# Kernel tuning notes

Measured on AMD Instinct MI355X. Metric: run time of the kernel, lower is better.

The kernel has to match this reference:

```python
import jax, jax.numpy as jnp
import numpy as np

DIM = 768
NUM_HEADS = 16
HEAD_DIM = DIM // NUM_HEADS


def setup_inputs() -> dict:
    key = jax.random.key(0)
    ks = jax.random.split(key, 9)
    B, S = 8, 1024
    s = 1.0 / np.sqrt(DIM)
    return {
        "x": jax.random.normal(ks[0], (B, S, DIM), dtype=jnp.float32),
        "Wq": jax.random.normal(ks[1], (DIM, DIM), dtype=jnp.float32) * s,
        "bq": jnp.zeros((DIM,), dtype=jnp.float32),
        "Wk": jax.random.normal(ks[2], (DIM, DIM), dtype=jnp.float32) * s,
        "bk": jnp.zeros((DIM,), dtype=jnp.float32),
        "Wv": jax.random.normal(ks[3], (DIM, DIM), dtype=jnp.float32) * s,
        "bv": jnp.zeros((DIM,), dtype=jnp.float32),
        "Wo": jax.random.normal(ks[4], (DIM, DIM), dtype=jnp.float32) * s,
        "bo": jnp.zeros((DIM,), dtype=jnp.float32),
    }


def reference(x, Wq, bq, Wk, bk, Wv, bv, Wo, bo):
    # x: [B, S, D]. Dropout in eval mode (identity).
    B, S, D = x.shape
    H, Hd = NUM_HEADS, HEAD_DIM
    # projections -> [B, H, S, Hd]
    q = (x @ Wq + bq).reshape(B, S, H, Hd).transpose(0, 2, 1, 3)
    k = (x @ Wk + bk).reshape(B, S, H, Hd).transpose(0, 2, 1, 3)
    v = (x @ Wv + bv).reshape(B, S, H, Hd).transpose(0, 2, 1, 3)
    scores = jnp.einsum('bhqd,bhkd->bhqk', q, k) / jnp.sqrt(jnp.asarray(Hd, x.dtype))
    attn = jax.nn.softmax(scores, axis=-1)
    out = jnp.einsum('bhqk,bhkd->bhqd', attn, v)  # [B, H, S, Hd]
    out = out.transpose(0, 2, 1, 3).reshape(B, S, D)
    return out @ Wo + bo
```

## Files before the change

kernel.cpp:

```cpp
#include <hip/hip_runtime.h>
#include <hip/hip_bf16.h>
#include <math.h>

#define DIM 768
#define HEADS 16
#define HD 48
#define BATCH 8
#define SEQ 1024
#define M_TOTAL (BATCH * SEQ)

using short8 = __attribute__((ext_vector_type(8))) short;
using f32x4 = __attribute__((ext_vector_type(4))) float;
using ushort8 = __attribute__((ext_vector_type(8))) unsigned short;
using ushort4v = __attribute__((ext_vector_type(4))) unsigned short;

__device__ __forceinline__ unsigned short f2bf(float f) {
    unsigned int u = __float_as_uint(f);
    u = u + 0x7FFFu + ((u >> 16) & 1u);
    return (unsigned short)(u >> 16);
}

__device__ __forceinline__ void load16_lds(const void* g, void* l) {
    __builtin_amdgcn_global_load_lds(
        (const __attribute__((address_space(1))) unsigned int*)g,
        (__attribute__((address_space(3))) unsigned int*)l, 16, 0, 0);
}

__device__ __forceinline__ ushort4v pk4bf(const f32x4 v) {
    union { __hip_bfloat162 h2[2]; ushort4v u4; } cv;
    cv.h2[0] = __float22bfloat162_rn(make_float2(v[0], v[1]));
    cv.h2[1] = __float22bfloat162_rn(make_float2(v[2], v[3]));
    return cv.u4;
}

__device__ __forceinline__ short8 cat44(ushort4v lo, ushort4v hi) {
    short8 r;
    r[0] = lo[0]; r[1] = lo[1]; r[2] = lo[2]; r[3] = lo[3];
    r[4] = hi[0]; r[5] = hi[1]; r[6] = hi[2]; r[7] = hi[3];
    return r;
}

__global__ __launch_bounds__(256)
void convert_bf16_kernel(const float* __restrict__ in, unsigned short* __restrict__ out) {
    const int idx = blockIdx.x * 256 + threadIdx.x;
    const float4* p = (const float4*)in + (size_t)idx * 2;
    const float4 a = p[0], b = p[1];
    ushort8 o;
    o[0] = f2bf(a.x); o[1] = f2bf(a.y); o[2] = f2bf(a.z); o[3] = f2bf(a.w);
    o[4] = f2bf(b.x); o[5] = f2bf(b.y); o[6] = f2bf(b.z); o[7] = f2bf(b.w);
    *((ushort8*)out + idx) = o;
}

__global__ __launch_bounds__(256)
void fill_vt_ones_kernel(unsigned short* __restrict__ vt) {
    const int g = blockIdx.x * 256 + threadIdx.x;
    const int bh = g >> 11;
    const int within = g & 2047;
    ushort8 o;
#pragma unroll
    for (int i = 0; i < 8; ++i) o[i] = 0x3F80;
    *(ushort8*)(vt + (size_t)bh * 65536 + 49152 + within * 8) = o;
}

__global__ __launch_bounds__(256)
void convert_w4_kernel(const float* __restrict__ W0, const float* __restrict__ W1,
                       const float* __restrict__ W2, const float* __restrict__ W3,
                       unsigned short* __restrict__ O0, unsigned short* __restrict__ O1,
                       unsigned short* __restrict__ O2, unsigned short* __restrict__ O3) {
    const float* W;
    unsigned short* O;
    switch (blockIdx.z) {
        case 0: W = W0; O = O0; break;
        case 1: W = W1; O = O1; break;
        case 2: W = W2; O = O2; break;
        default: W = W3; O = O3; break;
    }
    __shared__ unsigned short tile[32][33];
    const int t = threadIdx.x;
    const int r = t >> 3;
    const int c4 = (t & 7) * 4;
    {
        const float4 v = *(const float4*)(W + (size_t)(blockIdx.x * 32 + r) * DIM + blockIdx.y * 32 + c4);
        tile[r][c4 + 0] = f2bf(v.x);
        tile[r][c4 + 1] = f2bf(v.y);
        tile[r][c4 + 2] = f2bf(v.z);
        tile[r][c4 + 3] = f2bf(v.w);
    }
    __syncthreads();
    ushort4v o;
    o[0] = tile[c4 + 0][r];
    o[1] = tile[c4 + 1][r];
    o[2] = tile[c4 + 2][r];
    o[3] = tile[c4 + 3][r];
    *(ushort4v*)(O + (size_t)(blockIdx.y * 32 + r) * DIM + blockIdx.x * 32 + c4) = o;
}

__global__ __launch_bounds__(256)
void gemm_qkv_kernel(const unsigned short* __restrict__ A,
                     const unsigned short* __restrict__ Bt,
                     const float* __restrict__ bq, const float* __restrict__ bk,
                     const float* __restrict__ bv,
                     unsigned short* __restrict__ qp, unsigned short* __restrict__ kp,
                     unsigned short* __restrict__ vt) {
    __shared__ unsigned short As[128 * 32];
    __shared__ unsigned short Bs[128 * 32];

    const int tid = threadIdx.x;
    const int lane = tid & 63;
    const int w = tid >> 6;
    const int quad = lane >> 4;
    const int l15 = lane & 15;
    const int wr = (w >> 1) * 64;
    const int wc = (w & 1) * 64;
    const int row0 = blockIdx.x * 128;
    const int col0g = blockIdx.y * 128;

    const int sr = lane >> 2;
    const int sb = (lane & 3) * 16;

    f32x4 acc[4][4];
    const f32x4 zero = {0.f, 0.f, 0.f, 0.f};
#pragma unroll
    for (int i = 0; i < 4; ++i)
#pragma unroll
        for (int j = 0; j < 4; ++j) acc[i][j] = zero;

    const char* Abase = (const char*)A + (size_t)(row0 + 32 * w + sr) * (DIM * 2) + sb;
    const char* Bbase = (const char*)Bt + (size_t)(col0g + 32 * w + sr) * (DIM * 2) + sb;
    unsigned short* Al = As + w * 1024;
    unsigned short* Bl = Bs + w * 1024;

    for (int k0 = 0; k0 < DIM; k0 += 32) {
        __syncthreads();
        {
            const size_t kb = (size_t)k0 * 2;
            load16_lds(Abase + kb, Al);
            load16_lds(Abase + kb + (size_t)16 * DIM * 2, Al + 512);
            load16_lds(Bbase + kb, Bl);
            load16_lds(Bbase + kb + (size_t)16 * DIM * 2, Bl + 512);
        }
        __syncthreads();

        short8 af[4], bf[4];
        const int koff = quad * 8;
#pragma unroll
        for (int i = 0; i < 4; ++i)
            af[i] = *(const short8*)(As + (wr + 16 * i + l15) * 32 + koff);
#pragma unroll
        for (int j = 0; j < 4; ++j)
            bf[j] = *(const short8*)(Bs + (wc + 16 * j + l15) * 32 + koff);
#pragma unroll
        for (int i = 0; i < 4; ++i)
#pragma unroll
            for (int j = 0; j < 4; ++j)
                acc[i][j] = __builtin_amdgcn_mfma_f32_16x16x32_bf16(af[i], bf[j], acc[i][j], 0, 0, 0);
    }

    const int mat = blockIdx.y / 6;
    const int colbase = (blockIdx.y % 6) * 128;
    const float* bias = (mat == 0) ? bq : (mat == 1) ? bk : bv;
    const float sc = (mat == 0) ? (0.14433756729740643f * 1.4426950408889634f) : 1.0f;
#pragma unroll
    for (int j = 0; j < 4; ++j) {
        const int col = colbase + wc + 16 * j + l15;
        const float bj = bias[col];
        const int h = col / 48;
        const int d = col - h * 48;
        if (mat != 2) {
            unsigned short* outp = (mat == 0) ? qp : kp;
#pragma unroll
            for (int i = 0; i < 4; ++i) {
                const int row = row0 + wr + 16 * i + quad * 4;
#pragma unroll
                for (int r = 0; r < 4; ++r) {
                    const int b = (row + r) >> 10;
                    const int s = (row + r) & 1023;
                    outp[(((size_t)(b * 16 + h) * 1024 + s) << 6) + d] = f2bf((acc[i][j][r] + bj) * sc);
                }
            }
        } else {
#pragma unroll
            for (int i = 0; i < 4; ++i) {
                const int row = row0 + wr + 16 * i + quad * 4;
                const int b = row >> 10;
                const int s = row & 1023;
                ushort4v pk;
#pragma unroll
                for (int r = 0; r < 4; ++r) pk[r] = f2bf(acc[i][j][r] + bj);
                *(ushort4v*)&vt[(((size_t)(b * 16 + h) * 64 + d) << 10) + s] = pk;
            }
        }
    }
}

__global__ __launch_bounds__(256)
void gemm_out_kernel(const unsigned short* __restrict__ A,
                     const unsigned short* __restrict__ Bt,
                     const float* __restrict__ bias,
                     float* __restrict__ Out) {
    __shared__ unsigned short As[128 * 32];
    __shared__ unsigned short Bs[128 * 32];

    const int tid = threadIdx.x;
    const int lane = tid & 63;
    const int w = tid >> 6;
    const int quad = lane >> 4;
    const int l15 = lane & 15;
    const int wr = (w >> 1) * 64;
    const int wc = (w & 1) * 64;
    const int row0 = blockIdx.x * 128;
    const int col0 = blockIdx.y * 128;

    const int sr = lane >> 2;
    const int sb = (lane & 3) * 16;

    f32x4 acc[4][4];
    const f32x4 zero = {0.f, 0.f, 0.f, 0.f};
#pragma unroll
    for (int i = 0; i < 4; ++i)
#pragma unroll
        for (int j = 0; j < 4; ++j) acc[i][j] = zero;

    const char* Abase = (const char*)A + (size_t)(row0 + 32 * w + sr) * (DIM * 2) + sb;
    const char* Bbase = (const char*)Bt + (size_t)(col0 + 32 * w + sr) * (DIM * 2) + sb;
    unsigned short* Al = As + w * 1024;
    unsigned short* Bl = Bs + w * 1024;

    for (int k0 = 0; k0 < DIM; k0 += 32) {
        __syncthreads();
        {
            const size_t kb = (size_t)k0 * 2;
            load16_lds(Abase + kb, Al);
            load16_lds(Abase + kb + (size_t)16 * DIM * 2, Al + 512);
            load16_lds(Bbase + kb, Bl);
            load16_lds(Bbase + kb + (size_t)16 * DIM * 2, Bl + 512);
        }
        __syncthreads();

        short8 af[4], bf[4];
        const int koff = quad * 8;
#pragma unroll
        for (int i = 0; i < 4; ++i)
            af[i] = *(const short8*)(As + (wr + 16 * i + l15) * 32 + koff);
#pragma unroll
        for (int j = 0; j < 4; ++j)
            bf[j] = *(const short8*)(Bs + (wc + 16 * j + l15) * 32 + koff);
#pragma unroll
        for (int i = 0; i < 4; ++i)
#pragma unroll
            for (int j = 0; j < 4; ++j)
                acc[i][j] = __builtin_amdgcn_mfma_f32_16x16x32_bf16(af[i], bf[j], acc[i][j], 0, 0, 0);
    }

#pragma unroll
    for (int j = 0; j < 4; ++j) {
        const int col = col0 + wc + 16 * j + l15;
        const float bj = bias[col];
#pragma unroll
        for (int i = 0; i < 4; ++i) {
            const int row = row0 + wr + 16 * i + quad * 4;
#pragma unroll
            for (int r = 0; r < 4; ++r)
                Out[(size_t)(row + r) * DIM + col] = acc[i][j][r] + bj;
        }
    }
}

__global__ __launch_bounds__(256, 4)
void attn_mfma_kernel(const unsigned short* __restrict__ qp,
                      const unsigned short* __restrict__ kp,
                      const unsigned short* __restrict__ vt,
                      unsigned short* __restrict__ aob) {
    __shared__ unsigned short Ks[64 * 64];
    __shared__ unsigned short Vs[64 * 64];
    __shared__ unsigned short Ps[128 * 64];

    const int tid = threadIdx.x;
    const int lane = tid & 63;
    const int w = tid >> 6;
    const int quad = lane >> 4;
    const int l15 = lane & 15;
    const int sx = l15 & 7;
    const int wr = 32 * w;

    const int qt = blockIdx.x;
    const int h = blockIdx.y;
    const int b = blockIdx.z;
    const int bh = b * 16 + h;

    const unsigned short* qbase = qp + (((size_t)bh * 1024 + qt * 128) << 6);
    const unsigned short* kbase = kp + ((size_t)bh << 16);
    const unsigned short* vbase = vt + ((size_t)bh << 16);

    short8 qf[2][2];
#pragma unroll
    for (int i = 0; i < 2; ++i)
#pragma unroll
        for (int kb = 0; kb < 2; ++kb)
            qf[i][kb] = *(const short8*)(qbase + ((wr + 16 * i + l15) << 6) + kb * 32 + quad * 8);

    f32x4 of[2][4];
    const f32x4 zero = {0.f, 0.f, 0.f, 0.f};
#pragma unroll
    for (int i = 0; i < 2; ++i)
#pragma unroll
        for (int dj = 0; dj < 4; ++dj) of[i][dj] = zero;

    const int srow = lane >> 3;
    const int scol = lane & 7;
    const int r0 = w * 16 + srow;

    short8 kpre[2], vpre[2];
#pragma unroll
    for (int p = 0; p < 2; ++p) {
        const int row = r0 + p * 8;
        kpre[p] = *(const short8*)(kbase + ((size_t)row << 6) + scol * 8);
        vpre[p] = *(const short8*)(vbase + ((size_t)row << 10) + scol * 8);
    }

    for (int kt = 0; kt < SEQ / 64; ++kt) {
        __syncthreads();
#pragma unroll
        for (int p = 0; p < 2; ++p) {
            const int row = r0 + p * 8;
            const int sw = scol ^ (row & 7);
            *(short8*)(Ks + row * 64 + sw * 8) = kpre[p];
            *(short8*)(Vs + row * 64 + sw * 8) = vpre[p];
        }
        __syncthreads();
        if (kt + 1 < SEQ / 64) {
#pragma unroll
            for (int p = 0; p < 2; ++p) {
                const int row = r0 + p * 8;
                kpre[p] = *(const short8*)(kbase + ((size_t)((kt + 1) * 64 + row) << 6) + scol * 8);
                vpre[p] = *(const short8*)(vbase + ((size_t)row << 10) + (kt + 1) * 64 + scol * 8);
            }
        }

        f32x4 s[2][4];
#pragma unroll
        for (int j = 0; j < 4; ++j) {
            const int krow = 16 * j + l15;
            const short8 ka = *(const short8*)(Ks + krow * 64 + ((quad ^ sx) * 8));
            const short8 kb_ = *(const short8*)(Ks + krow * 64 + (((4 + quad) ^ sx) * 8));
            s[0][j] = __builtin_amdgcn_mfma_f32_16x16x32_bf16(ka, qf[0][0], zero, 0, 0, 0);
            s[0][j] = __builtin_amdgcn_mfma_f32_16x16x32_bf16(kb_, qf[0][1], s[0][j], 0, 0, 0);
            s[1][j] = __builtin_amdgcn_mfma_f32_16x16x32_bf16(ka, qf[1][0], zero, 0, 0, 0);
            s[1][j] = __builtin_amdgcn_mfma_f32_16x16x32_bf16(kb_, qf[1][1], s[1][j], 0, 0, 0);
        }

#pragma unroll
        for (int i = 0; i < 2; ++i) {
            const int rowq = wr + 16 * i + l15;
#pragma unroll
            for (int j = 0; j < 4; ++j) {
#pragma unroll
                for (int r = 0; r < 4; ++r) s[i][j][r] = __builtin_amdgcn_exp2f(s[i][j][r]);
                const int u = 4 * j + quad;
                const int su = u ^ l15;
                *(ushort4v*)(Ps + rowq * 64 + (su << 2)) = pk4bf(s[i][j]);
            }
        }

        short8 pf[2][2];
#pragma unroll
        for (int i = 0; i < 2; ++i) {
            const int rowq = wr + 16 * i + l15;
#pragma unroll
            for (int kb = 0; kb < 2; ++kb) {
                const int u0 = 8 * kb + 2 * quad;
                const ushort4v lo = *(const ushort4v*)(Ps + rowq * 64 + (((u0) ^ l15) << 2));
                const ushort4v hi = *(const ushort4v*)(Ps + rowq * 64 + (((u0 + 1) ^ l15) << 2));
                pf[i][kb] = cat44(lo, hi);
            }
        }
#pragma unroll
        for (int dj = 0; dj < 4; ++dj) {
            short8 vf0, vf1;
            {
                const int row = 16 * dj + l15;
                vf0 = *(const short8*)(Vs + row * 64 + (((quad) ^ sx) * 8));
                vf1 = *(const short8*)(Vs + row * 64 + (((4 + quad) ^ sx) * 8));
            }
#pragma unroll
            for (int i = 0; i < 2; ++i) {
                of[i][dj] = __builtin_amdgcn_mfma_f32_16x16x32_bf16(pf[i][0], vf0, of[i][dj], 0, 0, 0);
                of[i][dj] = __builtin_amdgcn_mfma_f32_16x16x32_bf16(pf[i][1], vf1, of[i][dj], 0, 0, 0);
            }
        }
    }

#pragma unroll
    for (int i = 0; i < 2; ++i)
#pragma unroll
        for (int r = 0; r < 4; ++r) {
            const float inv = 1.0f / of[i][3][r];
            const int srow_g = qt * 128 + wr + 16 * i + quad * 4 + r;
            const size_t rowoff = (size_t)(b * 1024 + srow_g) * DIM + h * 48 + l15;
#pragma unroll
            for (int dj = 0; dj < 3; ++dj)
                aob[rowoff + 16 * dj] = f2bf(of[i][dj][r] * inv);
        }
}

extern "C" void kernel_launch(void* const* d_in, const int* in_sizes, int n_in,
                              void* d_out, int out_size, void* d_ws, size_t ws_size,
                              hipStream_t stream) {
    const float* x  = (const float*)d_in[0];
    const float* Wq = (const float*)d_in[1];
    const float* bq = (const float*)d_in[2];
    const float* Wk = (const float*)d_in[3];
    const float* bk = (const float*)d_in[4];
    const float* Wv = (const float*)d_in[5];
    const float* bv = (const float*)d_in[6];
    const float* Wo = (const float*)d_in[7];
    const float* bo = (const float*)d_in[8];
    float* out = (float*)d_out;

    const size_t NELEM = (size_t)M_TOTAL * DIM;
    const size_t WELEM = (size_t)DIM * DIM;
    const size_t PELEM = (size_t)BATCH * HEADS * SEQ * 64;

    unsigned short* qpb = (unsigned short*)d_ws;
    unsigned short* kpb = qpb + PELEM;
    unsigned short* vtb = kpb + PELEM;
    unsigned short* xb  = vtb + PELEM;
    unsigned short* aob = xb + NELEM;
    unsigned short* wqkv = aob + NELEM;
    unsigned short* wob  = wqkv + 3 * WELEM;

    hipMemsetAsync(qpb, 0, PELEM * 2, stream);
    hipMemsetAsync(kpb, 0, PELEM * 2, stream);
    fill_vt_ones_kernel<<<1024, 256, 0, stream>>>(vtb);

    const int cvt_blocks = (int)(NELEM / 2048);
    convert_bf16_kernel<<<cvt_blocks, 256, 0, stream>>>(x, xb);
    convert_w4_kernel<<<dim3(24, 24, 4), 256, 0, stream>>>(
        Wq, Wk, Wv, Wo, wqkv, wqkv + WELEM, wqkv + 2 * WELEM, wob);

    gemm_qkv_kernel<<<dim3(M_TOTAL / 128, 18), 256, 0, stream>>>(
        xb, wqkv, bq, bk, bv, qpb, kpb, vtb);

    attn_mfma_kernel<<<dim3(SEQ / 128, HEADS, BATCH), 256, 0, stream>>>(qpb, kpb, vtb, aob);

    gemm_out_kernel<<<dim3(M_TOTAL / 128, DIM / 128), 256, 0, stream>>>(aob, wob, bo, out);
}
```

Before: 226.7 us.

## Fuse padding fills into QKV GEMM epilogue and deepen GEMM K-step

Removes the two full memsets of the padded Q/K buffers and the separate ones-fill kernel for V^T. Instead, the QKV GEMM epilogue writes the zero padding for Q/K and the ones rows for V^T only for the heads that block touches. Both GEMMs now load two 32-wide K slices per barrier pair, which halves the number of synchronisations, and they set a minimum of 4 blocks per CU via launch bounds. The cost is double the LDS per block, plus a fill whose coverage depends on several blocks writing each head's padding redundantly.

```diff
diff --git a/kernel.cpp b/kernel.cpp
--- a/kernel.cpp
+++ b/kernel.cpp
@@ -49,17 +49,6 @@
     o[0] = f2bf(a.x); o[1] = f2bf(a.y); o[2] = f2bf(a.z); o[3] = f2bf(a.w);
     o[4] = f2bf(b.x); o[5] = f2bf(b.y); o[6] = f2bf(b.z); o[7] = f2bf(b.w);
     *((ushort8*)out + idx) = o;
-}
-
-__global__ __launch_bounds__(256)
-void fill_vt_ones_kernel(unsigned short* __restrict__ vt) {
-    const int g = blockIdx.x * 256 + threadIdx.x;
-    const int bh = g >> 11;
-    const int within = g & 2047;
-    ushort8 o;
-#pragma unroll
-    for (int i = 0; i < 8; ++i) o[i] = 0x3F80;
-    *(ushort8*)(vt + (size_t)bh * 65536 + 49152 + within * 8) = o;
 }
 
 __global__ __launch_bounds__(256)
@@ -95,15 +84,15 @@
     *(ushort4v*)(O + (size_t)(blockIdx.y * 32 + r) * DIM + blockIdx.x * 32 + c4) = o;
 }
 
-__global__ __launch_bounds__(256)
+__global__ __launch_bounds__(256, 4)
 void gemm_qkv_kernel(const unsigned short* __restrict__ A,
                      const unsigned short* __restrict__ Bt,
                      const float* __restrict__ bq, const float* __restrict__ bk,
                      const float* __restrict__ bv,
                      unsigned short* __restrict__ qp, unsigned short* __restrict__ kp,
                      unsigned short* __restrict__ vt) {
-    __shared__ unsigned short As[128 * 32];
-    __shared__ unsigned short Bs[128 * 32];
+    __shared__ unsigned short As[2][128 * 32];
+    __shared__ unsigned short Bs[2][128 * 32];
 
     const int tid = threadIdx.x;
     const int lane = tid & 63;
@@ -127,33 +116,37 @@
 
     const char* Abase = (const char*)A + (size_t)(row0 + 32 * w + sr) * (DIM * 2) + sb;
     const char* Bbase = (const char*)Bt + (size_t)(col0g + 32 * w + sr) * (DIM * 2) + sb;
-    unsigned short* Al = As + w * 1024;
-    unsigned short* Bl = Bs + w * 1024;
-
-    for (int k0 = 0; k0 < DIM; k0 += 32) {
+
+    for (int k0 = 0; k0 < DIM; k0 += 64) {
         __syncthreads();
         {
             const size_t kb = (size_t)k0 * 2;
-            load16_lds(Abase + kb, Al);
-            load16_lds(Abase + kb + (size_t)16 * DIM * 2, Al + 512);
-            load16_lds(Bbase + kb, Bl);
-            load16_lds(Bbase + kb + (size_t)16 * DIM * 2, Bl + 512);
-        }
-        __syncthreads();
-
-        short8 af[4], bf[4];
+#pragma unroll
+            for (int p = 0; p < 2; ++p) {
+                load16_lds(Abase + kb + p * 64, As[p] + w * 1024);
+                load16_lds(Abase + kb + p * 64 + (size_t)16 * DIM * 2, As[p] + w * 1024 + 512);
+                load16_lds(Bbase + kb + p * 64, Bs[p] + w * 1024);
+                load16_lds(Bbase + kb + p * 64 + (size_t)16 * DIM * 2, Bs[p] + w * 1024 + 512);
+            }
+        }
+        __syncthreads();
+
         const int koff = quad * 8;
 #pragma unroll
-        for (int i = 0; i < 4; ++i)
-            af[i] = *(const short8*)(As + (wr + 16 * i + l15) * 32 + koff);
-#pragma unroll
-        for (int j = 0; j < 4; ++j)
-            bf[j] = *(const short8*)(Bs + (wc + 16 * j + l15) * 32 + koff);
-#pragma unroll
-        for (int i = 0; i < 4; ++i)
+        for (int p = 0; p < 2; ++p) {
+            short8 af[4], bf[4];
+#pragma unroll
+            for (int i = 0; i < 4; ++i)
+                af[i] = *(const short8*)(As[p] + (wr + 16 * i + l15) * 32 + koff);
 #pragma unroll
             for (int j = 0; j < 4; ++j)
-                acc[i][j] = __builtin_amdgcn_mfma_f32_16x16x32_bf16(af[i], bf[j], acc[i][j], 0, 0, 0);
+                bf[j] = *(const short8*)(Bs[p] + (wc + 16 * j + l15) * 32 + koff);
+#pragma unroll
+            for (int i = 0; i < 4; ++i)
+#pragma unroll
+                for (int j = 0; j < 4; ++j)
+                    acc[i][j] = __builtin_amdgcn_mfma_f32_16x16x32_bf16(af[i], bf[j], acc[i][j], 0, 0, 0);
+        }
     }
 
     const int mat = blockIdx.y / 6;
@@ -191,15 +184,37 @@
             }
         }
     }
-}
-
-__global__ __launch_bounds__(256)
+
+    if (mat != 2) {
+        unsigned short* outp = (mat == 0) ? qp : kp;
+        const int rowg = row0 + (tid >> 1);
+        const int bb = rowg >> 10;
+        const int ss = rowg & 1023;
+        ushort8 z;
+#pragma unroll
+        for (int i = 0; i < 8; ++i) z[i] = 0;
+        for (int h = (colbase + 47) / 48; 48 * h < colbase + 128; ++h)
+            *(ushort8*)&outp[(((size_t)(bb * 16 + h) * 1024 + ss) << 6) + 48 + (tid & 1) * 8] = z;
+    } else {
+        const int b0 = row0 >> 10;
+        const int s0 = row0 & 1023;
+        const int dd = 48 + (tid >> 4);
+        const int sc8 = (tid & 15) * 8;
+        ushort8 one;
+#pragma unroll
+        for (int i = 0; i < 8; ++i) one[i] = 0x3F80;
+        for (int h = (colbase + 47) / 48; 48 * h < colbase + 128; ++h)
+            *(ushort8*)&vt[(((size_t)(b0 * 16 + h) * 64 + dd) << 10) + s0 + sc8] = one;
+    }
+}
+
+__global__ __launch_bounds__(256, 4)
 void gemm_out_kernel(const unsigned short* __restrict__ A,
                      const unsigned short* __restrict__ Bt,
                      const float* __restrict__ bias,
                      float* __restrict__ Out) {
-    __shared__ unsigned short As[128 * 32];
-    __shared__ unsigned short Bs[128 * 32];
+    __shared__ unsigned short As[2][128 * 32];
+    __shared__ unsigned short Bs[2][128 * 32];
 
     const int tid = threadIdx.x;
     const int lane = tid & 63;
@@ -223,33 +238,37 @@
 
     const char* Abase = (const char*)A + (size_t)(row0 + 32 * w + sr) * (DIM * 2) + sb;
     const char* Bbase = (const char*)Bt + (size_t)(col0 + 32 * w + sr) * (DIM * 2) + sb;
-    unsigned short* Al = As + w * 1024;
-    unsigned short* Bl = Bs + w * 1024;
-
-    for (int k0 = 0; k0 < DIM; k0 += 32) {
+
+    for (int k0 = 0; k0 < DIM; k0 += 64) {
         __syncthreads();
         {
             const size_t kb = (size_t)k0 * 2;
-            load16_lds(Abase + kb, Al);
-            load16_lds(Abase + kb + (size_t)16 * DIM * 2, Al + 512);
-            load16_lds(Bbase + kb, Bl);
-            load16_lds(Bbase + kb + (size_t)16 * DIM * 2, Bl + 512);
-        }
-        __syncthreads();
-
-        short8 af[4], bf[4];
+#pragma unroll
+            for (int p = 0; p < 2; ++p) {
+                load16_lds(Abase + kb + p * 64, As[p] + w * 1024);
+                load16_lds(Abase + kb + p * 64 + (size_t)16 * DIM * 2, As[p] + w * 1024 + 512);
+                load16_lds(Bbase + kb + p * 64, Bs[p] + w * 1024);
+                load16_lds(Bbase + kb + p * 64 + (size_t)16 * DIM * 2, Bs[p] + w * 1024 + 512);
+            }
+        }
+        __syncthreads();
+
         const int koff = quad * 8;
 #pragma unroll
-        for (int i = 0; i < 4; ++i)
-            af[i] = *(const short8*)(As + (wr + 16 * i + l15) * 32 + koff);
-#pragma unroll
-        for (int j = 0; j < 4; ++j)
-            bf[j] = *(const short8*)(Bs + (wc + 16 * j + l15) * 32 + koff);
-#pragma unroll
-        for (int i = 0; i < 4; ++i)
+        for (int p = 0; p < 2; ++p) {
+            short8 af[4], bf[4];
+#pragma unroll
+            for (int i = 0; i < 4; ++i)
+                af[i] = *(const short8*)(As[p] + (wr + 16 * i + l15) * 32 + koff);
 #pragma unroll
             for (int j = 0; j < 4; ++j)
-                acc[i][j] = __builtin_amdgcn_mfma_f32_16x16x32_bf16(af[i], bf[j], acc[i][j], 0, 0, 0);
+                bf[j] = *(const short8*)(Bs[p] + (wc + 16 * j + l15) * 32 + koff);
+#pragma unroll
+            for (int i = 0; i < 4; ++i)
+#pragma unroll
+                for (int j = 0; j < 4; ++j)
+                    acc[i][j] = __builtin_amdgcn_mfma_f32_16x16x32_bf16(af[i], bf[j], acc[i][j], 0, 0, 0);
+        }
     }
 
 #pragma unroll
@@ -429,10 +448,6 @@
     unsigned short* wqkv = aob + NELEM;
     unsigned short* wob  = wqkv + 3 * WELEM;
 
-    hipMemsetAsync(qpb, 0, PELEM * 2, stream);
-    hipMemsetAsync(kpb, 0, PELEM * 2, stream);
-    fill_vt_ones_kernel<<<1024, 256, 0, stream>>>(vtb);
-
     const int cvt_blocks = (int)(NELEM / 2048);
     convert_bf16_kernel<<<cvt_blocks, 256, 0, stream>>>(x, xb);
     convert_w4_kernel<<<dim3(24, 24, 4), 256, 0, stream>>>(
```

Result: faster. 206.7 us (-8.8%).
